# Kernel tuning notes

Hardware: AMD Instinct MI355X
Metric: run time of the kernel (lower is better)

## Reference

```python
import jax, jax.numpy as jnp
import numpy as np

B, S, D, H = 4, 4096, 768, 8
BS = 64                # BigBird block size
NB = S // BS           # 64 blocks
NKB = 5                # key-block slots: global(0), prev, self, 2 random
HD = D // H
DFF = 4 * D
EPS = 1e-5


def _bigbird_pattern(seed=0):
    """Causal BigBird block pattern: per query block i attend to unique blocks
    {0, i-1, i, r1, r2} with r* random earlier blocks. Returns kb_idx [NB,NKB]
    and slot validity mask [NB,NKB]."""
    rng = np.random.RandomState(seed)
    kb = np.zeros((NB, NKB), np.int32)
    sm = np.zeros((NB, NKB), bool)
    for i in range(NB):
        blocks = []
        for b in (0, i - 1, i):
            if b >= 0 and b not in blocks:
                blocks.append(b)
        cand = [b for b in range(1, i - 1) if b not in blocks]
        n_r = min(NKB - len(blocks), 2, len(cand))
        if n_r > 0:
            blocks += list(rng.choice(cand, size=n_r, replace=False))
        for s, b in enumerate(blocks):
            kb[i, s] = b
            sm[i, s] = True
    return kb, sm


def setup_inputs() -> dict:
    key = jax.random.key(0)
    ks = jax.random.split(key, 12)
    init = lambda k, shape: jax.random.normal(k, shape, jnp.float32) * 0.02
    kb, sm = _bigbird_pattern()
    qpos = np.arange(BS)
    diag = (kb == np.arange(NB)[:, None])                      # slot == self block
    causal = qpos[:, None] >= qpos[None, :]                    # within-block causal
    mask = sm[:, None, :, None] & (~diag[:, None, :, None] | causal[None, :, None, :])
    return {
        "q": jax.random.normal(ks[0], (B, S, D), jnp.float32),
        "Wq": init(ks[1], (D, D)), "bq": jnp.zeros((D,), jnp.float32),
        "Wk": init(ks[2], (D, D)), "bk": jnp.zeros((D,), jnp.float32),
        "Wv": init(ks[3], (D, D)), "bv": jnp.zeros((D,), jnp.float32),
        "Wo": init(ks[4], (D, D)), "bo": jnp.zeros((D,), jnp.float32),
        "ln_g": jnp.ones((D,), jnp.float32), "ln_b": jnp.zeros((D,), jnp.float32),
        "W1": init(ks[5], (D, DFF)), "b1": jnp.zeros((DFF,), jnp.float32),
        "W2": init(ks[6], (DFF, D)), "b2": jnp.zeros((D,), jnp.float32),
        "kb_idx": jnp.asarray(kb, jnp.int32),
        "attn_mask": jnp.asarray(mask),                        # [NB,BS,NKB,BS] bool
    }


def _ln(x, g, b):
    m = jnp.mean(x, -1, keepdims=True)
    v = jnp.mean((x - m) ** 2, -1, keepdims=True)
    return (x - m) * jax.lax.rsqrt(v + EPS) * g + b


def reference(q, Wq, bq, Wk, bk, Wv, bv, Wo, bo, ln_g, ln_b, W1, b1, W2, b2, kb_idx, attn_mask):
    x = q
    # pre-norm residual: x + BigBirdAttn(ln(x)) (dropout omitted: eval mode)
    h = _ln(x, ln_g, ln_b)
    split = lambda t: t.reshape(B, NB, BS, H, HD).transpose(0, 3, 1, 2, 4)  # [B,H,NB,BS,HD]
    qh = split(h @ Wq + bq)
    kh = split(h @ Wk + bk)
    vh = split(h @ Wv + bv)
    kg = jnp.take(kh, kb_idx, axis=2)   # gather key blocks  [B,H,NB,NKB,BS,HD]
    vg = jnp.take(vh, kb_idx, axis=2)
    scores = jnp.einsum('bhnqd,bhnspd->bhnqsp', qh, kg) / jnp.sqrt(jnp.float32(HD))
    scores = jnp.where(attn_mask[None, None], scores, jnp.float32(-1e9))
    probs = jax.nn.softmax(scores.reshape(B, H, NB, BS, NKB * BS), axis=-1).reshape(scores.shape)
    ctx = jnp.einsum('bhnqsp,bhnspd->bhnqd', probs, vg)       # [B,H,NB,BS,HD]
    ctx = ctx.transpose(0, 2, 3, 1, 4).reshape(B, S, D)
    x = x + (ctx @ Wo + bo)
    # pre-norm residual: x + FFN(ln(x)) (same ResidualConnection norm reused, as in source)
    h2 = _ln(x, ln_g, ln_b)
    ffn = jax.nn.relu(h2 @ W1 + b1) @ W2 + b2
    return x + ffn
```

## Files before the change

### kernel.cpp

```cpp
#include <hip/hip_runtime.h>
#include <math.h>

static constexpr int Bb   = 4;
static constexpr int Ss   = 4096;
static constexpr int Dd   = 768;
static constexpr int HDm  = 96;
static constexpr int DFFc = 3072;
static constexpr int MROWS = Bb * Ss;
static constexpr int NBK  = 64;
static constexpr int Hh   = 8;
static constexpr int QLD  = 2304;

typedef float f32x4_t __attribute__((ext_vector_type(4)));
typedef short s16x8_t __attribute__((ext_vector_type(8)));

__device__ __forceinline__ unsigned short f2bf(float f) {
  union { float f; unsigned int u; } c; c.f = f;
  unsigned int u = c.u;
  unsigned int r = (u + 0x7FFFu + ((u >> 16) & 1u)) >> 16;
  return (unsigned short)r;
}
__device__ __forceinline__ float bf2f(unsigned short u) {
  union { unsigned int u; float f; } c; c.u = ((unsigned int)u) << 16;
  return c.f;
}

__device__ __forceinline__ void gload16(const void* g, void* l) {
  __builtin_amdgcn_global_load_lds(
      (const __attribute__((address_space(1))) void*)g,
      (__attribute__((address_space(3))) void*)l, 16, 0, 0);
}

__global__ __launch_bounds__(256)
void transpose_cast(const float* __restrict__ src, unsigned short* __restrict__ dst,
                    int K, int N) {
  __shared__ float t[64][65];
  const int n0 = blockIdx.x * 64, k0 = blockIdx.y * 64;
  const int tid = threadIdx.x;
  {
    const int r = tid >> 2, cs = (tid & 3) * 16;
    const float* sp = src + (size_t)(k0 + r) * N + n0 + cs;
#pragma unroll
    for (int u = 0; u < 4; u++) {
      float4 v = *(const float4*)(sp + u * 4);
      t[r][cs + u * 4 + 0] = v.x; t[r][cs + u * 4 + 1] = v.y;
      t[r][cs + u * 4 + 2] = v.z; t[r][cs + u * 4 + 3] = v.w;
    }
  }
  __syncthreads();
  {
    const int n = tid >> 2, ks = (tid & 3) * 16;
    unsigned short o[16];
#pragma unroll
    for (int j = 0; j < 16; j++) o[j] = f2bf(t[ks + j][n]);
    unsigned short* dp = dst + (size_t)(n0 + n) * K + k0 + ks;
    *(uint4*)(dp)     = *(uint4*)(o);
    *(uint4*)(dp + 8) = *(uint4*)(o + 8);
  }
}

__global__ __launch_bounds__(192)
void ln_kernel(const float* __restrict__ x, const float* __restrict__ g,
               const float* __restrict__ beta, unsigned short* __restrict__ out) {
  const int row = blockIdx.x;
  const int t = threadIdx.x;
  const float* xr = x + (size_t)row * Dd;
  float4 v = *(const float4*)(xr + t * 4);
  float s  = v.x + v.y + v.z + v.w;
  float sq = v.x * v.x + v.y * v.y + v.z * v.z + v.w * v.w;
#pragma unroll
  for (int o = 32; o; o >>= 1) {
    s  += __shfl_xor(s, o);
    sq += __shfl_xor(sq, o);
  }
  __shared__ float rs[4], rq[4];
  const int w = t >> 6;
  if ((t & 63) == 0) { rs[w] = s; rq[w] = sq; }
  __syncthreads();
  s  = rs[0] + rs[1] + rs[2];
  sq = rq[0] + rq[1] + rq[2];
  const float mean = s * (1.0f / Dd);
  const float var  = sq * (1.0f / Dd) - mean * mean;
  const float rstd = rsqrtf(var + 1e-5f);
  float4 gv = *(const float4*)(g + t * 4);
  float4 bv = *(const float4*)(beta + t * 4);
  ushort4 o;
  o.x = f2bf((v.x - mean) * rstd * gv.x + bv.x);
  o.y = f2bf((v.y - mean) * rstd * gv.y + bv.y);
  o.z = f2bf((v.z - mean) * rstd * gv.z + bv.z);
  o.w = f2bf((v.w - mean) * rstd * gv.w + bv.w);
  *(ushort4*)(out + (size_t)row * Dd + t * 4) = o;
}

template <int RELU, int OUTBF16, int RESID, int SEL3>
__global__ __launch_bounds__(256)
void bgemm(const unsigned short* __restrict__ A, const unsigned short* __restrict__ Bt,
           const float* __restrict__ b0, const float* __restrict__ b1,
           const float* __restrict__ b2, const float* __restrict__ resid,
           float* __restrict__ Cf, unsigned short* __restrict__ Cb,
           int N, int K, int lda, int GX) {
  __shared__ __align__(16) unsigned short lds[2][2][128][32];
  const int tid = threadIdx.x;

  const int nwg = gridDim.x;
  const int GYc = (nwg / GX) >> 3;
  const int xcd = blockIdx.x & 7;
  const int t0  = blockIdx.x >> 3;
  const int bxg = t0 / (6 * GYc);
  const int rr_ = t0 - bxg * 6 * GYc;
  const int by  = xcd * GYc + rr_ / 6;
  const int bx  = bxg * 6 + rr_ % 6;
  const int n0 = bx * 128, m0 = by * 128;

  const int lane = tid & 63, w = tid >> 6;
  const int wr = (w >> 1) * 64, wc = (w & 1) * 64;
  const int fr = lane & 15, fq = lane >> 4;
  const int l4 = lane >> 2, lc = (lane & 3) * 8;

  const unsigned short* Ab = A + (size_t)(m0 + w * 32 + l4) * lda + lc;
  const unsigned short* Bb2 = Bt + (size_t)(n0 + w * 32 + l4) * K + lc;
  const size_t a16 = (size_t)16 * lda, b16 = (size_t)16 * K;

  f32x4_t acc[4][4];
#pragma unroll
  for (int i = 0; i < 4; i++)
#pragma unroll
    for (int j = 0; j < 4; j++) acc[i][j] = (f32x4_t)0.0f;

  const int NT = K >> 5;
  int cur = 0;
  gload16(Ab,        &lds[0][0][w * 32][0]);
  gload16(Ab + a16,  &lds[0][0][w * 32 + 16][0]);
  gload16(Bb2,       &lds[0][1][w * 32][0]);
  gload16(Bb2 + b16, &lds[0][1][w * 32 + 16][0]);
  __syncthreads();

  for (int t = 0; t < NT; t++) {
    if (t + 1 < NT) {
      const int ko = (t + 1) << 5;
      gload16(Ab + ko,        &lds[cur ^ 1][0][w * 32][0]);
      gload16(Ab + a16 + ko,  &lds[cur ^ 1][0][w * 32 + 16][0]);
      gload16(Bb2 + ko,       &lds[cur ^ 1][1][w * 32][0]);
      gload16(Bb2 + b16 + ko, &lds[cur ^ 1][1][w * 32 + 16][0]);
    }
    s16x8_t af[4], bf[4];
#pragma unroll
    for (int i = 0; i < 4; i++)
      af[i] = *(const s16x8_t*)&lds[cur][0][wr + i * 16 + fr][fq * 8];
#pragma unroll
    for (int j = 0; j < 4; j++)
      bf[j] = *(const s16x8_t*)&lds[cur][1][wc + j * 16 + fr][fq * 8];
#pragma unroll
    for (int i = 0; i < 4; i++)
#pragma unroll
      for (int j = 0; j < 4; j++)
        acc[i][j] = __builtin_amdgcn_mfma_f32_16x16x32_bf16(af[i], bf[j],
                                                            acc[i][j], 0, 0, 0);
    __syncthreads();
    cur ^= 1;
  }

  constexpr int CLD = 76;
  float* cs = (float*)(&lds[0][0][0][0]) + w * (16 * CLD);

#pragma unroll
  for (int i = 0; i < 4; i++) {
#pragma unroll
    for (int j = 0; j < 4; j++) {
      const int col = n0 + wc + j * 16 + fr;
      float bc;
      if (SEL3)
        bc = col < 768 ? b0[col] : (col < 1536 ? b1[col - 768] : b2[col - 1536]);
      else
        bc = b0[col];
#pragma unroll
      for (int r4 = 0; r4 < 4; r4++) {
        float v = acc[i][j][r4] + bc;
        if (RELU) v = fmaxf(v, 0.0f);
        cs[(fq * 4 + r4) * CLD + j * 16 + fr] = v;
      }
    }
    if (OUTBF16) {
#pragma unroll
      for (int u = 0; u < 2; u++) {
        const int rr = (lane >> 3) + u * 8;
        const int c0 = (lane & 7) * 8;
        float4 x0 = *(float4*)&cs[rr * CLD + c0];
        float4 x1 = *(float4*)&cs[rr * CLD + c0 + 4];
        unsigned short o[8];
        o[0] = f2bf(x0.x); o[1] = f2bf(x0.y); o[2] = f2bf(x0.z); o[3] = f2bf(x0.w);
        o[4] = f2bf(x1.x); o[5] = f2bf(x1.y); o[6] = f2bf(x1.z); o[7] = f2bf(x1.w);
        *(uint4*)(Cb + (size_t)(m0 + wr + i * 16 + rr) * N + n0 + wc + c0) =
            *(uint4*)o;
      }
    } else {
#pragma unroll
      for (int u = 0; u < 4; u++) {
        const int rr = (lane >> 4) + u * 4;
        const int c0 = (lane & 15) * 4;
        const size_t off = (size_t)(m0 + wr + i * 16 + rr) * N + n0 + wc + c0;
        float4 x = *(float4*)&cs[rr * CLD + c0];
        if (RESID) {
          float4 r = *(const float4*)(resid + off);
          x.x += r.x; x.y += r.y; x.z += r.z; x.w += r.w;
        }
        *(float4*)(Cf + off) = x;
      }
    }
    __syncthreads();
  }
}

__global__ __launch_bounds__(256)
void attn_mfma(const unsigned short* __restrict__ qkv,
               const int* __restrict__ kbidx,
               unsigned short* __restrict__ ctx) {
  const int bid = blockIdx.x;
  const int n = bid & 63;
  const int h = (bid >> 6) & 7;
  const int b = bid >> 9;
  const int tid = threadIdx.x;
  const int w = tid >> 6, lane = tid & 63;
  const int fr = lane & 15, fq = lane >> 4;

  __shared__ __align__(16) unsigned short Ks[64][104];
  __shared__ __align__(16) unsigned short Vt[96][72];
  __shared__ __align__(16) unsigned short Ps[64][72];

  s16x8_t qa[3];
  {
    const unsigned short* qrow =
        qkv + ((size_t)(b * Ss) + n * 64 + w * 16 + fr) * QLD + h * HDm;
#pragma unroll
    for (int kq = 0; kq < 3; kq++)
      qa[kq] = *(const s16x8_t*)(qrow + kq * 32 + fq * 8);
  }

  f32x4_t o_acc[6];
#pragma unroll
  for (int dt = 0; dt < 6; dt++) o_acc[dt] = (f32x4_t)0.0f;
  float m_run[4] = {-1e30f, -1e30f, -1e30f, -1e30f};
  float l_run[4] = {0.0f, 0.0f, 0.0f, 0.0f};
  const float scale = 0.1020620726f;

  for (int s = 0; s < 5; s++) {
    const int kb = kbidx[n * 5 + s];
    if (!(s == 0 || kb != 0)) continue;
    const bool diag = (kb == n);

    __syncthreads();
    {
      const unsigned short* kbase =
          qkv + 768 + ((size_t)(b * Ss) + kb * 64) * QLD + h * HDm;
#pragma unroll
      for (int u = 0; u < 3; u++) {
        const int c = tid + 256 * u;
        const int row = c / 12, d0 = (c % 12) * 8;
        *(uint4*)&Ks[row][d0] = *(const uint4*)(kbase + (size_t)row * QLD + d0);
      }
    }
    {
      const unsigned short* vbase =
          qkv + 1536 + ((size_t)(b * Ss) + kb * 64 + lane) * QLD + h * HDm + w * 24;
      unsigned short va[24];
      *(uint4*)&va[0]  = *(const uint4*)(vbase);
      *(uint4*)&va[8]  = *(const uint4*)(vbase + 8);
      *(uint4*)&va[16] = *(const uint4*)(vbase + 16);
#pragma unroll
      for (int j = 0; j < 24; j++) Vt[w * 24 + j][lane] = va[j];
    }
    __syncthreads();

    f32x4_t sf[4];
#pragma unroll
    for (int jt = 0; jt < 4; jt++) {
      sf[jt] = (f32x4_t)0.0f;
#pragma unroll
      for (int kq = 0; kq < 3; kq++) {
        s16x8_t kf = *(const s16x8_t*)&Ks[jt * 16 + fr][kq * 32 + fq * 8];
        sf[jt] = __builtin_amdgcn_mfma_f32_16x16x32_bf16(qa[kq], kf, sf[jt], 0, 0, 0);
      }
    }

    float p[4][4];
    float mt[4] = {-1e30f, -1e30f, -1e30f, -1e30f};
#pragma unroll
    for (int jt = 0; jt < 4; jt++)
#pragma unroll
      for (int r = 0; r < 4; r++) {
        float v = sf[jt][r] * scale;
        if (diag && (jt * 16 + fr) > (w * 16 + fq * 4 + r)) v = -1e9f;
        p[jt][r] = v;
        mt[r] = fmaxf(mt[r], v);
      }
#pragma unroll
    for (int off = 1; off < 16; off <<= 1)
#pragma unroll
      for (int r = 0; r < 4; r++) mt[r] = fmaxf(mt[r], __shfl_xor(mt[r], off));
    float fsc[4], rs[4];
#pragma unroll
    for (int r = 0; r < 4; r++) {
      const float mnew = fmaxf(m_run[r], mt[r]);
      fsc[r] = __expf(m_run[r] - mnew);
      m_run[r] = mnew;
      float s0 = 0.0f;
#pragma unroll
      for (int jt = 0; jt < 4; jt++) {
        p[jt][r] = __expf(p[jt][r] - mnew);
        s0 += p[jt][r];
      }
      rs[r] = s0;
    }
#pragma unroll
    for (int off = 1; off < 16; off <<= 1)
#pragma unroll
      for (int r = 0; r < 4; r++) rs[r] += __shfl_xor(rs[r], off);
#pragma unroll
    for (int r = 0; r < 4; r++) l_run[r] = l_run[r] * fsc[r] + rs[r];
#pragma unroll
    for (int dt = 0; dt < 6; dt++)
#pragma unroll
      for (int r = 0; r < 4; r++) o_acc[dt][r] *= fsc[r];

#pragma unroll
    for (int jt = 0; jt < 4; jt++)
#pragma unroll
      for (int r = 0; r < 4; r++)
        Ps[w * 16 + fq * 4 + r][jt * 16 + fr] = f2bf(p[jt][r]);

    s16x8_t pf[2];
#pragma unroll
    for (int k2 = 0; k2 < 2; k2++)
      pf[k2] = *(const s16x8_t*)&Ps[w * 16 + fr][k2 * 32 + fq * 8];
#pragma unroll
    for (int dt = 0; dt < 6; dt++)
#pragma unroll
      for (int k2 = 0; k2 < 2; k2++) {
        s16x8_t vf = *(const s16x8_t*)&Vt[dt * 16 + fr][k2 * 32 + fq * 8];
        o_acc[dt] = __builtin_amdgcn_mfma_f32_16x16x32_bf16(pf[k2], vf, o_acc[dt], 0, 0, 0);
      }
  }

#pragma unroll
  for (int r = 0; r < 4; r++) {
    const float inv = 1.0f / l_run[r];
    unsigned short* dst =
        ctx + ((size_t)(b * Ss) + n * 64 + w * 16 + fq * 4 + r) * QLD + h * HDm;
#pragma unroll
    for (int dt = 0; dt < 6; dt++)
      dst[dt * 16 + fr] = f2bf(o_acc[dt][r] * inv);
  }
}

extern "C" void kernel_launch(void* const* d_in, const int* in_sizes, int n_in,
                              void* d_out, int out_size, void* d_ws, size_t ws_size,
                              hipStream_t stream) {
  const float* x    = (const float*)d_in[0];
  const float* Wq   = (const float*)d_in[1];
  const float* bq   = (const float*)d_in[2];
  const float* Wk   = (const float*)d_in[3];
  const float* bk   = (const float*)d_in[4];
  const float* Wv   = (const float*)d_in[5];
  const float* bv   = (const float*)d_in[6];
  const float* Wo   = (const float*)d_in[7];
  const float* bo   = (const float*)d_in[8];
  const float* ln_g = (const float*)d_in[9];
  const float* ln_b = (const float*)d_in[10];
  const float* W1   = (const float*)d_in[11];
  const float* b1   = (const float*)d_in[12];
  const float* W2   = (const float*)d_in[13];
  const float* b2   = (const float*)d_in[14];
  const int*   kb   = (const int*)d_in[15];

  float* out = (float*)d_out;
  unsigned short* ws = (unsigned short*)d_ws;

  constexpr size_t WSQ = (size_t)Dd * Dd;
  unsigned short* WqkvT = ws;
  unsigned short* Wot   = WqkvT + 3 * WSQ;
  unsigned short* W1t   = Wot + WSQ;
  unsigned short* W2t   = W1t + (size_t)Dd * DFFc;
  unsigned short* h     = W2t + (size_t)Dd * DFFc;
  unsigned short* pool  = h + (size_t)MROWS * Dd;
  unsigned short* fused = pool;
  unsigned short* fbuf  = pool;

  transpose_cast<<<dim3(12, 12), 256, 0, stream>>>(Wq, WqkvT,           Dd, Dd);
  transpose_cast<<<dim3(12, 12), 256, 0, stream>>>(Wk, WqkvT + WSQ,     Dd, Dd);
  transpose_cast<<<dim3(12, 12), 256, 0, stream>>>(Wv, WqkvT + 2 * WSQ, Dd, Dd);
  transpose_cast<<<dim3(12, 12), 256, 0, stream>>>(Wo, Wot,             Dd, Dd);
  transpose_cast<<<dim3(48, 12), 256, 0, stream>>>(W1, W1t, Dd, DFFc);
  transpose_cast<<<dim3(12, 48), 256, 0, stream>>>(W2, W2t, DFFc, Dd);

  ln_kernel<<<MROWS, 192, 0, stream>>>(x, ln_g, ln_b, h);

  bgemm<0, 1, 0, 1><<<2304, 256, 0, stream>>>(
      h, WqkvT, bq, bk, bv, nullptr, nullptr, fused, QLD, Dd, Dd, 18);

  attn_mfma<<<Bb * Hh * NBK, 256, 0, stream>>>(fused, kb, fused);

  bgemm<0, 0, 1, 0><<<768, 256, 0, stream>>>(
      fused, Wot, bo, nullptr, nullptr, x, out, nullptr, Dd, Dd, QLD, 6);

  ln_kernel<<<MROWS, 192, 0, stream>>>(out, ln_g, ln_b, h);

  bgemm<1, 1, 0, 0><<<3072, 256, 0, stream>>>(
      h, W1t, b1, nullptr, nullptr, nullptr, nullptr, fbuf, DFFc, Dd, Dd, 24);

  bgemm<0, 0, 1, 0><<<768, 256, 0, stream>>>(
      fbuf, W2t, b2, nullptr, nullptr, out, out, nullptr, Dd, DFFc, DFFc, 6);
}
```

Measured before the change: 567.1 us.

## Use triple-buffered LDS ring with one barrier per k-step in bf16 GEMM

Replaces the GEMM main loop's double-buffered LDS with a three-slot ring that keeps two k-tiles of global-to-LDS loads in flight. Each iteration waits only until the oldest stage has landed (vmcnt(4)), then issues one barrier before computing. The goal is to hide global load latency and remove the trailing __syncthreads from each iteration. In exchange, LDS use per block grows by half, which may reduce occupancy. Correctness now depends on the hand-written waitcnt matching the number of loads gload16 issues.

```diff
diff --git a/kernel.cpp b/kernel.cpp
--- a/kernel.cpp
+++ b/kernel.cpp
@@ -99,7 +99,7 @@
            const float* __restrict__ b2, const float* __restrict__ resid,
            float* __restrict__ Cf, unsigned short* __restrict__ Cb,
            int N, int K, int lda, int GX) {
-  __shared__ __align__(16) unsigned short lds[2][2][128][32];
+  __shared__ __align__(16) unsigned short ring[3][2][128][32];
   const int tid = threadIdx.x;
 
   const int nwg = gridDim.x;
@@ -128,40 +128,55 @@
     for (int j = 0; j < 4; j++) acc[i][j] = (f32x4_t)0.0f;
 
   const int NT = K >> 5;
-  int cur = 0;
-  gload16(Ab,        &lds[0][0][w * 32][0]);
-  gload16(Ab + a16,  &lds[0][0][w * 32 + 16][0]);
-  gload16(Bb2,       &lds[0][1][w * 32][0]);
-  gload16(Bb2 + b16, &lds[0][1][w * 32 + 16][0]);
+
+#define STAGE(kt, slot)                                         \
+  {                                                             \
+    const int ko_ = (kt) << 5;                                  \
+    gload16(Ab + ko_,        &ring[slot][0][w * 32][0]);        \
+    gload16(Ab + a16 + ko_,  &ring[slot][0][w * 32 + 16][0]);   \
+    gload16(Bb2 + ko_,       &ring[slot][1][w * 32][0]);        \
+    gload16(Bb2 + b16 + ko_, &ring[slot][1][w * 32 + 16][0]);   \
+  }
+
+#define COMPUTE(slot)                                                          \
+  {                                                                            \
+    s16x8_t af[4], bf[4];                                                      \
+    _Pragma("unroll") for (int i = 0; i < 4; i++)                              \
+        af[i] = *(const s16x8_t*)&ring[slot][0][wr + i * 16 + fr][fq * 8];     \
+    _Pragma("unroll") for (int j = 0; j < 4; j++)                              \
+        bf[j] = *(const s16x8_t*)&ring[slot][1][wc + j * 16 + fr][fq * 8];     \
+    _Pragma("unroll") for (int i = 0; i < 4; i++)                              \
+        _Pragma("unroll") for (int j = 0; j < 4; j++)                          \
+            acc[i][j] = __builtin_amdgcn_mfma_f32_16x16x32_bf16(af[i], bf[j],  \
+                                                                acc[i][j], 0, 0, 0); \
+  }
+
+  STAGE(0, 0);
+  STAGE(1, 1);
+
+  int rb = 0;
+  for (int t = 0; t < NT - 1; t++) {
+    asm volatile("s_waitcnt vmcnt(4)" ::: "memory");
+    __builtin_amdgcn_s_barrier();
+    asm volatile("" ::: "memory");
+    if (t + 2 < NT) {
+      int nb = rb + 2; if (nb >= 3) nb -= 3;
+      STAGE(t + 2, nb);
+    }
+    COMPUTE(rb);
+    rb = (rb + 1 == 3) ? 0 : rb + 1;
+  }
+  asm volatile("s_waitcnt vmcnt(0)" ::: "memory");
+  __builtin_amdgcn_s_barrier();
+  asm volatile("" ::: "memory");
+  COMPUTE(rb);
   __syncthreads();
 
-  for (int t = 0; t < NT; t++) {
-    if (t + 1 < NT) {
-      const int ko = (t + 1) << 5;
-      gload16(Ab + ko,        &lds[cur ^ 1][0][w * 32][0]);
-      gload16(Ab + a16 + ko,  &lds[cur ^ 1][0][w * 32 + 16][0]);
-      gload16(Bb2 + ko,       &lds[cur ^ 1][1][w * 32][0]);
-      gload16(Bb2 + b16 + ko, &lds[cur ^ 1][1][w * 32 + 16][0]);
-    }
-    s16x8_t af[4], bf[4];
-#pragma unroll
-    for (int i = 0; i < 4; i++)
-      af[i] = *(const s16x8_t*)&lds[cur][0][wr + i * 16 + fr][fq * 8];
-#pragma unroll
-    for (int j = 0; j < 4; j++)
-      bf[j] = *(const s16x8_t*)&lds[cur][1][wc + j * 16 + fr][fq * 8];
-#pragma unroll
-    for (int i = 0; i < 4; i++)
-#pragma unroll
-      for (int j = 0; j < 4; j++)
-        acc[i][j] = __builtin_amdgcn_mfma_f32_16x16x32_bf16(af[i], bf[j],
-                                                            acc[i][j], 0, 0, 0);
-    __syncthreads();
-    cur ^= 1;
-  }
+#undef STAGE
+#undef COMPUTE
 
   constexpr int CLD = 76;
-  float* cs = (float*)(&lds[0][0][0][0]) + w * (16 * CLD);
+  float* cs = (float*)(&ring[0][0][0][0]) + w * (16 * CLD);
 
 #pragma unroll
   for (int i = 0; i < 4; i++) {
```

Measured after the change: 533.1 us. 1.06x faster.
